# Kernel tuning notes

Hardware: AMD Instinct MI355X
Metric: run time of the kernel (lower is better)

## Reference

```python
import jax, jax.numpy as jnp
import numpy as np

BS, C, H, W = 4, 128, 64, 64  # input_dim=128
INNER = 64


def setup_inputs() -> dict:
    key = jax.random.key(0)
    ks = jax.random.split(key, 9)
    s_in = 1.0 / np.sqrt(C)
    s_inner = 1.0 / np.sqrt(INNER)
    return {
        "inpt": jax.random.normal(ks[0], (BS, C, H, W), dtype=jnp.float32),
        "Wq": jax.random.normal(ks[1], (INNER, C), dtype=jnp.float32) * s_in,
        "bq": jax.random.normal(ks[2], (INNER,), dtype=jnp.float32) * 0.01,
        "Wk": jax.random.normal(ks[3], (INNER, C), dtype=jnp.float32) * s_in,
        "bk": jax.random.normal(ks[4], (INNER,), dtype=jnp.float32) * 0.01,
        "Wv": jax.random.normal(ks[5], (INNER, C), dtype=jnp.float32) * s_in,
        "bv": jax.random.normal(ks[6], (INNER,), dtype=jnp.float32) * 0.01,
        "Wo": jax.random.normal(ks[7], (C, INNER), dtype=jnp.float32) * s_inner,
        "bo": jax.random.normal(ks[8], (C,), dtype=jnp.float32) * 0.01,
    }


def reference(inpt, Wq, bq, Wk, bk, Wv, bv, Wo, bo):
    bs, c, h, w = inpt.shape
    L = h * w
    # [bs, C, H, W] -> [bs, L, C] (tokens = spatial positions)
    x = inpt.reshape(bs, c, L).transpose(0, 2, 1)
    q = jnp.einsum('blc,dc->bld', x, Wq) + bq  # [bs, L, INNER]
    k = jnp.einsum('blc,dc->bld', x, Wk) + bk
    v = jnp.einsum('blc,dc->bld', x, Wv) + bv
    # torch code divides by np.round(sqrt(d), 2); for d=64 this is exactly 8.0
    scale = jnp.float32(np.round(np.sqrt(q.shape[-1]), 2))
    scores = jnp.einsum('bld,bmd->blm', q, k) / scale  # [bs, L, L] score matrix
    factors = jax.nn.softmax(scores, axis=-1)
    ctx = jnp.einsum('blm,bmd->bld', factors, v)  # [bs, L, INNER]
    out = jnp.einsum('bld,cd->blc', ctx, Wo) + bo  # [bs, L, C]
    out = out.transpose(0, 2, 1).reshape(bs, c, h, w)
    return inpt + out
```

## Files before the change

kernel.cpp:

```cpp
#include <hip/hip_runtime.h>
#include <hip/hip_bf16.h>

typedef __bf16 bf16x8 __attribute__((ext_vector_type(8)));
typedef __bf16 bf16x4 __attribute__((ext_vector_type(4)));
typedef short  s16x4  __attribute__((ext_vector_type(4)));
typedef float  f32x4  __attribute__((ext_vector_type(4)));

#define MFMA32(a, b, c) __builtin_amdgcn_mfma_f32_16x16x32_bf16((a), (b), (c), 0, 0, 0)
#define MFMA16K(a, b, c) __builtin_amdgcn_mfma_f32_16x16x16bf16_1k((a), (b), (c), 0, 0, 0)

#if __has_builtin(__builtin_amdgcn_exp2f)
#define EXP2F(x) __builtin_amdgcn_exp2f(x)
#else
#define EXP2F(x) __expf(0.6931471805599453f * (x))
#endif

#define GL16(G, L)                                                            \
    __builtin_amdgcn_global_load_lds(                                         \
        (const __attribute__((address_space(1))) void*)(G),                   \
        (__attribute__((address_space(3))) void*)(L), 16, 0, 0)

#define SPLIT 8
#define QSCALE 0.18033688011112042f
#define BBOUND 12.0f


__global__ __launch_bounds__(256) void qkv_kernel(
    const float* __restrict__ inpt,
    const float* __restrict__ Wq, const float* __restrict__ bq,
    const float* __restrict__ Wk, const float* __restrict__ bk,
    const float* __restrict__ Wv, const float* __restrict__ bv,
    __bf16* __restrict__ Qws, __bf16* __restrict__ Kws, __bf16* __restrict__ VTws)
{
    __shared__ __align__(16) __bf16 xT[16 * 140];
    __shared__ __align__(16) __bf16 os[16 * 144];
    const int bid = blockIdx.x;
    const int b   = bid >> 8;
    const int l0  = (bid & 255) << 4;
    const int t   = threadIdx.x;

    {
        const int c = t >> 1, half = t & 1;
        const float* xin = inpt + ((size_t)(b * 128 + c)) * 4096 + l0 + half * 8;
        float4 v0 = *(const float4*)xin;
        float4 v1 = *(const float4*)(xin + 4);
        const int tok0 = half * 8;
        xT[(tok0 + 0) * 140 + c] = (__bf16)v0.x;
        xT[(tok0 + 1) * 140 + c] = (__bf16)v0.y;
        xT[(tok0 + 2) * 140 + c] = (__bf16)v0.z;
        xT[(tok0 + 3) * 140 + c] = (__bf16)v0.w;
        xT[(tok0 + 4) * 140 + c] = (__bf16)v1.x;
        xT[(tok0 + 5) * 140 + c] = (__bf16)v1.y;
        xT[(tok0 + 6) * 140 + c] = (__bf16)v1.z;
        xT[(tok0 + 7) * 140 + c] = (__bf16)v1.w;
    }
    __syncthreads();

    const int w    = t >> 6;
    const int lane = t & 63;
    const int quad = lane >> 4;
    const int l15  = lane & 15;

    f32x4 acc[3];
    #pragma unroll
    for (int j = 0; j < 3; ++j)
        #pragma unroll
        for (int r = 0; r < 4; ++r) acc[j][r] = 0.f;

    #pragma unroll
    for (int ks = 0; ks < 4; ++ks) {
        bf16x8 af = *(const bf16x8*)&xT[l15 * 140 + ks * 32 + quad * 8];
        #pragma unroll
        for (int j = 0; j < 3; ++j) {
            const int wn   = w * 3 + j;
            const int msel = wn >> 2;
            const float* W = (msel == 0) ? Wq : ((msel == 1) ? Wk : Wv);
            const float* Wp = W + ((wn & 3) * 16 + l15) * 128 + ks * 32 + quad * 8;
            float4 wa = *(const float4*)Wp;
            float4 wb = *(const float4*)(Wp + 4);
            bf16x8 bf;
            bf[0] = (__bf16)wa.x; bf[1] = (__bf16)wa.y;
            bf[2] = (__bf16)wa.z; bf[3] = (__bf16)wa.w;
            bf[4] = (__bf16)wb.x; bf[5] = (__bf16)wb.y;
            bf[6] = (__bf16)wb.z; bf[7] = (__bf16)wb.w;
            acc[j] = MFMA32(af, bf, acc[j]);
        }
    }

    #pragma unroll
    for (int j = 0; j < 3; ++j) {
        const int wn   = w * 3 + j;
        const int msel = wn >> 2;
        const int o0   = (wn & 3) * 16;
        const float* bb = (msel == 0) ? bq : ((msel == 1) ? bk : bv);
        float bias = bb[o0 + l15];
        if (msel < 2) {
            const float scl = (msel == 0) ? QSCALE : 1.0f;
            const int oc = wn * 16 + l15;
            #pragma unroll
            for (int r = 0; r < 4; ++r)
                os[(quad * 4 + r) * 144 + oc] = (__bf16)((acc[j][r] + bias) * scl);
        } else {
            const int d  = o0 + l15;
            const int kt = l0 >> 6;
            const int kc = (l0 >> 4) & 3;
            bf16x4 v;
            #pragma unroll
            for (int r = 0; r < 4; ++r) v[r] = (__bf16)(acc[j][r] + bias);
            *(bf16x4*)(VTws + (size_t)b * 262144 + kt * 4096
                       + d * 64 + quad * 16 + kc * 4) = v;
        }
    }
    __syncthreads();

    {
        const int tok = t >> 4, c = t & 15;
        bf16x8 v = *(const bf16x8*)&os[tok * 144 + c * 8];
        if (c < 8) {
            *(bf16x8*)(Qws + ((size_t)(b * 4096 + l0 + tok)) * 64 + c * 8) = v;
        } else {
            const int d8 = c - 8;
            __bf16* dst = Kws + (size_t)b * 262144
                + (l0 >> 6) * 4096
                + ((l0 >> 4) & 3) * 1024
                + (d8 >> 2) * 512
                + (d8 & 3) * 128
                + tok * 8;
            *(bf16x8*)dst = v;
        }
    }
}

__global__ __launch_bounds__(256, 4) void attn_kernel(
    const __bf16* __restrict__ Qws, const __bf16* __restrict__ Kws,
    const __bf16* __restrict__ VTws,
    __bf16* __restrict__ Ops, float* __restrict__ Lws)
{
    __shared__ __align__(16) __bf16 sbuf[2][8192];

    const int bid   = blockIdx.x;
    const int split = bid >> 7;
    const int qi    = bid & 127;
    const int b  = qi >> 5;
    const int l0 = (qi & 31) << 7;
    const int t    = threadIdx.x;
    const int w    = t >> 6;
    const int lane = t & 63;
    const int quad = lane >> 4;
    const int l15  = lane & 15;

    bf16x8 qf[2][2];
    #pragma unroll
    for (int qs = 0; qs < 2; ++qs) {
        const __bf16* qptr = Qws
            + ((size_t)(b * 4096 + l0 + w * 32 + qs * 16 + l15)) * 64 + quad * 8;
        qf[qs][0] = *(const bf16x8*)qptr;
        qf[qs][1] = *(const bf16x8*)(qptr + 32);
    }

    f32x4 cfr[2][4];
    #pragma unroll
    for (int qs = 0; qs < 2; ++qs)
        #pragma unroll
        for (int mt = 0; mt < 4; ++mt)
            #pragma unroll
            for (int r = 0; r < 4; ++r) cfr[qs][mt][r] = 0.f;
    float l_acc[2] = {0.f, 0.f};

    int voff[8];
    #pragma unroll
    for (int mt = 0; mt < 4; ++mt) {
        const int d = mt * 16 + l15;
        #pragma unroll
        for (int kc8 = 0; kc8 < 2; ++kc8)
            voff[kc8 * 4 + mt] = d * 64 + (((2 * quad + kc8) ^ (d & 7)) * 8);
    }

    const uint4* Vg = (const uint4*)(VTws + ((size_t)b << 18));
    const int rw = t >> 3, cw = (t & 7) ^ ((t >> 3) & 7);
    const uint4* vbase = Vg + rw * 8 + cw + split * 4096;
    const uint4* kbase = (const uint4*)(Kws + ((size_t)b << 18))
                       + t + split * 4096;

    union B4 { bf16x4 h; s16x4 s; };
    union V8 { bf16x8 v; s16x4 q[2]; };

    auto stage = [&](int kt, int slot) {
        __bf16* Kd = &sbuf[slot][0];
        __bf16* Vd = &sbuf[slot][4096];
        const uint4* kp = kbase + kt * 512;
        const uint4* vp = vbase + kt * 512;
        GL16(kp,       Kd +        w * 512);
        GL16(kp + 256, Kd + 2048 + w * 512);
        GL16(vp,       Vd +        w * 512);
        GL16(vp + 256, Vd + 2048 + w * 512);
    };

    auto tile_step = [&](int slot) {
        const __bf16* Kb = &sbuf[slot][0];
        const __bf16* Vb = &sbuf[slot][4096];
        B4 pk[2][4];
        #pragma unroll
        for (int nt = 0; nt < 4; ++nt) {
            bf16x8 k0 = *(const bf16x8*)(Kb + nt * 1024 +       lane * 8);
            bf16x8 k1 = *(const bf16x8*)(Kb + nt * 1024 + 512 + lane * 8);
            #pragma unroll
            for (int qs = 0; qs < 2; ++qs) {
                f32x4 a = {-BBOUND, -BBOUND, -BBOUND, -BBOUND};
                a = MFMA32(k0, qf[qs][0], a);
                a = MFMA32(k1, qf[qs][1], a);
                float p0 = EXP2F(a[0]), p1 = EXP2F(a[1]);
                float p2 = EXP2F(a[2]), p3 = EXP2F(a[3]);
                pk[qs][nt].h[0] = (__bf16)p0; pk[qs][nt].h[1] = (__bf16)p1;
                pk[qs][nt].h[2] = (__bf16)p2; pk[qs][nt].h[3] = (__bf16)p3;
                l_acc[qs] += (p0 + p1) + (p2 + p3);
            }
        }
        __builtin_amdgcn_s_setprio(1);
        #pragma unroll
        for (int kc8 = 0; kc8 < 2; ++kc8) {
            #pragma unroll
            for (int mt = 0; mt < 4; ++mt) {
                V8 vv;
                vv.v = *(const bf16x8*)&Vb[voff[kc8 * 4 + mt]];
                #pragma unroll
                for (int qs = 0; qs < 2; ++qs) {
                    cfr[qs][mt] = MFMA16K(vv.q[0], pk[qs][2 * kc8 + 0].s, cfr[qs][mt]);
                    cfr[qs][mt] = MFMA16K(vv.q[1], pk[qs][2 * kc8 + 1].s, cfr[qs][mt]);
                }
            }
        }
        __builtin_amdgcn_s_setprio(0);
    };

    stage(0, 0);
    for (int h = 0; h < 8; ++h) {
        asm volatile("s_waitcnt vmcnt(0)" ::: "memory");
        __builtin_amdgcn_s_barrier();
        asm volatile("" ::: "memory");
        if (h < 7) stage(h + 1, (h + 1) & 1);
        tile_step(h & 1);
    }

    __builtin_amdgcn_s_barrier();
    asm volatile("" ::: "memory");

    {
        __bf16* tb = (__bf16*)sbuf + w * 2176;
        #pragma unroll
        for (int qs = 0; qs < 2; ++qs)
            #pragma unroll
            for (int mt = 0; mt < 4; ++mt) {
                bf16x4 v;
                #pragma unroll
                for (int r = 0; r < 4; ++r) v[r] = (__bf16)cfr[qs][mt][r];
                *(bf16x4*)&tb[(qs * 16 + l15) * 68 + mt * 16 + quad * 4] = v;
            }
        const int rowbase = (split * 4 + b) * 4096 + l0 + w * 32;
        #pragma unroll
        for (int hh = 0; hh < 4; ++hh) {
            const int chunk = lane + hh * 64;
            const int tok = chunk >> 3, c8 = chunk & 7;
            bf16x8 v = *(const bf16x8*)&tb[tok * 68 + c8 * 8];
            *(bf16x8*)(Ops + (size_t)(rowbase + tok) * 64 + c8 * 8) = v;
        }
        #pragma unroll
        for (int qs = 0; qs < 2; ++qs) {
            float lr = l_acc[qs];
            lr += __shfl_xor(lr, 16);
            lr += __shfl_xor(lr, 32);
            if (quad == 0) Lws[rowbase + qs * 16 + l15] = lr;
        }
    }
}

__global__ __launch_bounds__(256) void outproj_kernel(
    const float* __restrict__ inpt,
    const __bf16* __restrict__ Ops, const float* __restrict__ Lws,
    const float* __restrict__ Wo, const float* __restrict__ bo,
    float* __restrict__ out)
{
    __shared__ __align__(16) __bf16 cx[16 * 72];
    const int bid = blockIdx.x;
    const int b   = bid >> 8;
    const int l0  = (bid & 255) << 4;
    const int t   = threadIdx.x;

    {
        const int token = t >> 4, d4 = (t & 15) << 2;
        const int rowb  = b * 4096 + l0 + token;
        float denom = 0.f;
        #pragma unroll
        for (int s = 0; s < SPLIT; ++s) denom += Lws[s * 16384 + rowb];
        const float inv = 1.f / denom;
        float ax = 0.f, ay = 0.f, az = 0.f, aw = 0.f;
        #pragma unroll
        for (int s = 0; s < SPLIT; ++s) {
            const bf16x4 v = *(const bf16x4*)(Ops
                + ((size_t)(s * 16384 + rowb)) * 64 + d4);
            ax += (float)v[0]; ay += (float)v[1];
            az += (float)v[2]; aw += (float)v[3];
        }
        bf16x4 pv;
        pv[0] = (__bf16)(ax * inv); pv[1] = (__bf16)(ay * inv);
        pv[2] = (__bf16)(az * inv); pv[3] = (__bf16)(aw * inv);
        *(bf16x4*)&cx[token * 72 + d4] = pv;
    }
    __syncthreads();

    const int w    = t >> 6;
    const int lane = t & 63;
    const int quad = lane >> 4;
    const int l15  = lane & 15;

    f32x4 acc[2];
    #pragma unroll
    for (int mi = 0; mi < 2; ++mi)
        #pragma unroll
        for (int r = 0; r < 4; ++r) acc[mi][r] = 0.f;

    #pragma unroll
    for (int ks = 0; ks < 2; ++ks) {
        bf16x8 bfrag = *(const bf16x8*)&cx[l15 * 72 + ks * 32 + quad * 8];
        #pragma unroll
        for (int mi = 0; mi < 2; ++mi) {
            const int crow = (w * 2 + mi) * 16 + l15;
            const float* Wp = Wo + crow * 64 + ks * 32 + quad * 8;
            float4 wa = *(const float4*)Wp;
            float4 wb = *(const float4*)(Wp + 4);
            bf16x8 afrag;
            afrag[0] = (__bf16)wa.x; afrag[1] = (__bf16)wa.y;
            afrag[2] = (__bf16)wa.z; afrag[3] = (__bf16)wa.w;
            afrag[4] = (__bf16)wb.x; afrag[5] = (__bf16)wb.y;
            afrag[6] = (__bf16)wb.z; afrag[7] = (__bf16)wb.w;
            acc[mi] = MFMA32(afrag, bfrag, acc[mi]);
        }
    }

    #pragma unroll
    for (int mi = 0; mi < 2; ++mi) {
        #pragma unroll
        for (int r = 0; r < 4; ++r) {
            const int c = (w * 2 + mi) * 16 + quad * 4 + r;
            const size_t addr = ((size_t)(b * 128 + c)) * 4096 + l0 + l15;
            out[addr] = inpt[addr] + bo[c] + acc[mi][r];
        }
    }
}

extern "C" void kernel_launch(void* const* d_in, const int* in_sizes, int n_in,
                              void* d_out, int out_size, void* d_ws, size_t ws_size,
                              hipStream_t stream)
{
    const float* inpt = (const float*)d_in[0];
    const float* Wq   = (const float*)d_in[1];
    const float* bq   = (const float*)d_in[2];
    const float* Wk   = (const float*)d_in[3];
    const float* bk   = (const float*)d_in[4];
    const float* Wv   = (const float*)d_in[5];
    const float* bv   = (const float*)d_in[6];
    const float* Wo   = (const float*)d_in[7];
    const float* bo   = (const float*)d_in[8];
    float* out = (float*)d_out;

    char* ws = (char*)d_ws;
    const size_t MB = (size_t)1 << 20;
    __bf16* Qws  = (__bf16*)(ws + 0 * MB);
    __bf16* Kws  = (__bf16*)(ws + 2 * MB);
    __bf16* VTws = (__bf16*)(ws + 4 * MB);
    __bf16* Ops  = (__bf16*)(ws + 6 * MB);
    float*  Lws  = (float*)(ws + 24 * MB);

    qkv_kernel<<<1024, 256, 0, stream>>>(inpt, Wq, bq, Wk, bk, Wv, bv, Qws, Kws, VTws);
    attn_kernel<<<SPLIT * 128, 256, 0, stream>>>(Qws, Kws, VTws, Ops, Lws);
    outproj_kernel<<<1024, 256, 0, stream>>>(inpt, Ops, Lws, Wo, bo, out);
}
```

Before: 125.0 us.

## Pre-convert weights to bf16 and enlarge QKV/outproj token tiles to 64

Adds a small kernel that converts Wq/Wk/Wv/Wo to bf16 once per call into the workspace. The QKV and output-projection kernels now process 64 tokens per block instead of 16, so each weight fragment is reused across four token tiles rather than being reloaded and converted from fp32 per block. Grid sizes drop from 1024 to 256 blocks, which increases per-thread register use (12 accumulators in QKV) and adds an extra launch, at the risk of lower parallelism on a large GPU.

After: 118.5 us. 5.2% less time.

```diff
diff --git a/kernel.cpp b/kernel.cpp
--- a/kernel.cpp
+++ b/kernel.cpp
@@ -25,34 +25,51 @@
 #define BBOUND 12.0f
 
 
-__global__ __launch_bounds__(256) void qkv_kernel(
+__global__ __launch_bounds__(256) void wprep_kernel(
+    const float* __restrict__ Wq, const float* __restrict__ Wk,
+    const float* __restrict__ Wv, const float* __restrict__ Wo,
+    __bf16* __restrict__ Wqkv_b, __bf16* __restrict__ Wo_b)
+{
+    const int idx = (blockIdx.x * 256 + threadIdx.x) * 4;
+    const float* src;
+    __bf16* dst;
+    if (idx < 8192)       { src = Wq + idx;         dst = Wqkv_b + idx; }
+    else if (idx < 16384) { src = Wk + idx - 8192;  dst = Wqkv_b + idx; }
+    else if (idx < 24576) { src = Wv + idx - 16384; dst = Wqkv_b + idx; }
+    else                  { src = Wo + idx - 24576; dst = Wo_b + idx - 24576; }
+    float4 v = *(const float4*)src;
+    bf16x4 o;
+    o[0] = (__bf16)v.x; o[1] = (__bf16)v.y;
+    o[2] = (__bf16)v.z; o[3] = (__bf16)v.w;
+    *(bf16x4*)dst = o;
+}
+
+__global__ __launch_bounds__(256, 4) void qkv_kernel(
     const float* __restrict__ inpt,
-    const float* __restrict__ Wq, const float* __restrict__ bq,
-    const float* __restrict__ Wk, const float* __restrict__ bk,
-    const float* __restrict__ Wv, const float* __restrict__ bv,
+    const float* __restrict__ bq, const float* __restrict__ bk,
+    const float* __restrict__ bv,
+    const __bf16* __restrict__ Wqkv_b,
     __bf16* __restrict__ Qws, __bf16* __restrict__ Kws, __bf16* __restrict__ VTws)
 {
-    __shared__ __align__(16) __bf16 xT[16 * 140];
-    __shared__ __align__(16) __bf16 os[16 * 144];
+    __shared__ __align__(16) __bf16 xT[64 * 136];
+    __shared__ __align__(16) __bf16 os[64 * 136];
     const int bid = blockIdx.x;
-    const int b   = bid >> 8;
-    const int l0  = (bid & 255) << 4;
+    const int b   = bid >> 6;
+    const int l0  = (bid & 63) << 6;
     const int t   = threadIdx.x;
 
     {
         const int c = t >> 1, half = t & 1;
-        const float* xin = inpt + ((size_t)(b * 128 + c)) * 4096 + l0 + half * 8;
-        float4 v0 = *(const float4*)xin;
-        float4 v1 = *(const float4*)(xin + 4);
-        const int tok0 = half * 8;
-        xT[(tok0 + 0) * 140 + c] = (__bf16)v0.x;
-        xT[(tok0 + 1) * 140 + c] = (__bf16)v0.y;
-        xT[(tok0 + 2) * 140 + c] = (__bf16)v0.z;
-        xT[(tok0 + 3) * 140 + c] = (__bf16)v0.w;
-        xT[(tok0 + 4) * 140 + c] = (__bf16)v1.x;
-        xT[(tok0 + 5) * 140 + c] = (__bf16)v1.y;
-        xT[(tok0 + 6) * 140 + c] = (__bf16)v1.z;
-        xT[(tok0 + 7) * 140 + c] = (__bf16)v1.w;
+        const float* xin = inpt + ((size_t)(b * 128 + c)) * 4096 + l0 + half * 32;
+        #pragma unroll
+        for (int i = 0; i < 8; ++i) {
+            float4 v = *(const float4*)(xin + i * 4);
+            const int tok = half * 32 + i * 4;
+            xT[(tok + 0) * 136 + c] = (__bf16)v.x;
+            xT[(tok + 1) * 136 + c] = (__bf16)v.y;
+            xT[(tok + 2) * 136 + c] = (__bf16)v.z;
+            xT[(tok + 3) * 136 + c] = (__bf16)v.w;
+        }
     }
     __syncthreads();
 
@@ -61,71 +78,63 @@
     const int quad = lane >> 4;
     const int l15  = lane & 15;
 
-    f32x4 acc[3];
-    #pragma unroll
-    for (int j = 0; j < 3; ++j)
+    f32x4 acc[12];
+    #pragma unroll
+    for (int j = 0; j < 12; ++j)
         #pragma unroll
         for (int r = 0; r < 4; ++r) acc[j][r] = 0.f;
 
     #pragma unroll
     for (int ks = 0; ks < 4; ++ks) {
-        bf16x8 af = *(const bf16x8*)&xT[l15 * 140 + ks * 32 + quad * 8];
-        #pragma unroll
-        for (int j = 0; j < 3; ++j) {
-            const int wn   = w * 3 + j;
-            const int msel = wn >> 2;
-            const float* W = (msel == 0) ? Wq : ((msel == 1) ? Wk : Wv);
-            const float* Wp = W + ((wn & 3) * 16 + l15) * 128 + ks * 32 + quad * 8;
-            float4 wa = *(const float4*)Wp;
-            float4 wb = *(const float4*)(Wp + 4);
-            bf16x8 bf;
-            bf[0] = (__bf16)wa.x; bf[1] = (__bf16)wa.y;
-            bf[2] = (__bf16)wa.z; bf[3] = (__bf16)wa.w;
-            bf[4] = (__bf16)wb.x; bf[5] = (__bf16)wb.y;
-            bf[6] = (__bf16)wb.z; bf[7] = (__bf16)wb.w;
+        bf16x8 af = *(const bf16x8*)&xT[(w * 16 + l15) * 136 + ks * 32 + quad * 8];
+        #pragma unroll
+        for (int j = 0; j < 12; ++j) {
+            bf16x8 bf = *(const bf16x8*)(Wqkv_b + j * 2048 + l15 * 128
+                                         + ks * 32 + quad * 8);
             acc[j] = MFMA32(af, bf, acc[j]);
         }
     }
 
     #pragma unroll
-    for (int j = 0; j < 3; ++j) {
-        const int wn   = w * 3 + j;
-        const int msel = wn >> 2;
-        const int o0   = (wn & 3) * 16;
+    for (int j = 0; j < 12; ++j) {
+        const int msel = j >> 2;
+        const int o0   = (j & 3) * 16;
         const float* bb = (msel == 0) ? bq : ((msel == 1) ? bk : bv);
         float bias = bb[o0 + l15];
         if (msel < 2) {
             const float scl = (msel == 0) ? QSCALE : 1.0f;
-            const int oc = wn * 16 + l15;
+            const int oc = j * 16 + l15;
             #pragma unroll
             for (int r = 0; r < 4; ++r)
-                os[(quad * 4 + r) * 144 + oc] = (__bf16)((acc[j][r] + bias) * scl);
+                os[(w * 16 + quad * 4 + r) * 136 + oc]
+                    = (__bf16)((acc[j][r] + bias) * scl);
         } else {
             const int d  = o0 + l15;
-            const int kt = l0 >> 6;
-            const int kc = (l0 >> 4) & 3;
+            const int kt = bid & 63;
             bf16x4 v;
             #pragma unroll
             for (int r = 0; r < 4; ++r) v[r] = (__bf16)(acc[j][r] + bias);
             *(bf16x4*)(VTws + (size_t)b * 262144 + kt * 4096
-                       + d * 64 + quad * 16 + kc * 4) = v;
+                       + d * 64 + quad * 16 + w * 4) = v;
         }
     }
     __syncthreads();
 
-    {
-        const int tok = t >> 4, c = t & 15;
-        bf16x8 v = *(const bf16x8*)&os[tok * 144 + c * 8];
-        if (c < 8) {
-            *(bf16x8*)(Qws + ((size_t)(b * 4096 + l0 + tok)) * 64 + c * 8) = v;
+    #pragma unroll
+    for (int g = 0; g < 4; ++g) {
+        const int cid = t + g * 256;
+        const int tok = cid >> 4, c8 = cid & 15;
+        bf16x8 v = *(const bf16x8*)&os[tok * 136 + c8 * 8];
+        if (c8 < 8) {
+            *(bf16x8*)(Qws + ((size_t)(b * 4096 + l0 + tok)) * 64 + c8 * 8) = v;
         } else {
-            const int d8 = c - 8;
+            const int d8 = c8 - 8;
             __bf16* dst = Kws + (size_t)b * 262144
-                + (l0 >> 6) * 4096
-                + ((l0 >> 4) & 3) * 1024
+                + (bid & 63) * 4096
+                + (tok >> 4) * 1024
                 + (d8 >> 2) * 512
                 + (d8 & 3) * 128
-                + tok * 8;
+                + (tok & 15) * 8;
             *(bf16x8*)dst = v;
         }
     }
@@ -274,37 +283,41 @@
     }
 }
 
-__global__ __launch_bounds__(256) void outproj_kernel(
+__global__ __launch_bounds__(256, 4) void outproj_kernel(
     const float* __restrict__ inpt,
     const __bf16* __restrict__ Ops, const float* __restrict__ Lws,
-    const float* __restrict__ Wo, const float* __restrict__ bo,
+    const __bf16* __restrict__ Wo_b, const float* __restrict__ bo,
     float* __restrict__ out)
 {
-    __shared__ __align__(16) __bf16 cx[16 * 72];
+    __shared__ __align__(16) __bf16 cx[64 * 72];
     const int bid = blockIdx.x;
-    const int b   = bid >> 8;
-    const int l0  = (bid & 255) << 4;
+    const int b   = bid >> 6;
+    const int l0  = (bid & 63) << 6;
     const int t   = threadIdx.x;
 
     {
-        const int token = t >> 4, d4 = (t & 15) << 2;
+        const int token = t >> 2;
         const int rowb  = b * 4096 + l0 + token;
         float denom = 0.f;
         #pragma unroll
         for (int s = 0; s < SPLIT; ++s) denom += Lws[s * 16384 + rowb];
         const float inv = 1.f / denom;
-        float ax = 0.f, ay = 0.f, az = 0.f, aw = 0.f;
-        #pragma unroll
-        for (int s = 0; s < SPLIT; ++s) {
-            const bf16x4 v = *(const bf16x4*)(Ops
-                + ((size_t)(s * 16384 + rowb)) * 64 + d4);
-            ax += (float)v[0]; ay += (float)v[1];
-            az += (float)v[2]; aw += (float)v[3];
-        }
-        bf16x4 pv;
-        pv[0] = (__bf16)(ax * inv); pv[1] = (__bf16)(ay * inv);
-        pv[2] = (__bf16)(az * inv); pv[3] = (__bf16)(aw * inv);
-        *(bf16x4*)&cx[token * 72 + d4] = pv;
+        #pragma unroll
+        for (int g = 0; g < 4; ++g) {
+            const int d4 = (((t & 3) + g * 4)) << 2;
+            float ax = 0.f, ay = 0.f, az = 0.f, aw = 0.f;
+            #pragma unroll
+            for (int s = 0; s < SPLIT; ++s) {
+                const bf16x4 v = *(const bf16x4*)(Ops
+                    + ((size_t)(s * 16384 + rowb)) * 64 + d4);
+                ax += (float)v[0]; ay += (float)v[1];
+                az += (float)v[2]; aw += (float)v[3];
+            }
+            bf16x4 pv;
+            pv[0] = (__bf16)(ax * inv); pv[1] = (__bf16)(ay * inv);
+            pv[2] = (__bf16)(az * inv); pv[3] = (__bf16)(aw * inv);
+            *(bf16x4*)&cx[token * 72 + d4] = pv;
+        }
     }
     __syncthreads();
 
@@ -313,37 +326,42 @@
     const int quad = lane >> 4;
     const int l15  = lane & 15;
 
-    f32x4 acc[2];
+    f32x4 acc[2][4];
     #pragma unroll
     for (int mi = 0; mi < 2; ++mi)
         #pragma unroll
-        for (int r = 0; r < 4; ++r) acc[mi][r] = 0.f;
+        for (int nt = 0; nt < 4; ++nt)
+            #pragma unroll
+            for (int r = 0; r < 4; ++r) acc[mi][nt][r] = 0.f;
 
     #pragma unroll
     for (int ks = 0; ks < 2; ++ks) {
-        bf16x8 bfrag = *(const bf16x8*)&cx[l15 * 72 + ks * 32 + quad * 8];
+        bf16x8 bfr[4];
+        #pragma unroll
+        for (int nt = 0; nt < 4; ++nt)
+            bfr[nt] = *(const bf16x8*)&cx[(nt * 16 + l15) * 72 + ks * 32 + quad * 8];
         #pragma unroll
         for (int mi = 0; mi < 2; ++mi) {
             const int crow = (w * 2 + mi) * 16 + l15;
-            const float* Wp = Wo + crow * 64 + ks * 32 + quad * 8;
-            float4 wa = *(const float4*)Wp;
-            float4 wb = *(const float4*)(Wp + 4);
-            bf16x8 afrag;
-            afrag[0] = (__bf16)wa.x; afrag[1] = (__bf16)wa.y;
-            afrag[2] = (__bf16)wa.z; afrag[3] = (__bf16)wa.w;
-            afrag[4] = (__bf16)wb.x; afrag[5] = (__bf16)wb.y;
-            afrag[6] = (__bf16)wb.z; afrag[7] = (__bf16)wb.w;
-            acc[mi] = MFMA32(afrag, bfrag, acc[mi]);
+            bf16x8 af = *(const bf16x8*)(Wo_b + crow * 64 + ks * 32 + quad * 8);
+            #pragma unroll
+            for (int nt = 0; nt < 4; ++nt)
+                acc[mi][nt] = MFMA32(af, bfr[nt], acc[mi][nt]);
         }
     }
 
     #pragma unroll
     for (int mi = 0; mi < 2; ++mi) {
-        #pragma unroll
-        for (int r = 0; r < 4; ++r) {
-            const int c = (w * 2 + mi) * 16 + quad * 4 + r;
-            const size_t addr = ((size_t)(b * 128 + c)) * 4096 + l0 + l15;
-            out[addr] = inpt[addr] + bo[c] + acc[mi][r];
+        const int c0 = (w * 2 + mi) * 16 + quad * 4;
+        #pragma unroll
+        for (int nt = 0; nt < 4; ++nt) {
+            #pragma unroll
+            for (int r = 0; r < 4; ++r) {
+                const int c = c0 + r;
+                const size_t addr = ((size_t)(b * 128 + c)) * 4096
+                                  + l0 + nt * 16 + l15;
+                out[addr] = inpt[addr] + bo[c] + acc[mi][nt][r];
+            }
         }
     }
 }
@@ -365,13 +383,16 @@
 
     char* ws = (char*)d_ws;
     const size_t MB = (size_t)1 << 20;
-    __bf16* Qws  = (__bf16*)(ws + 0 * MB);
-    __bf16* Kws  = (__bf16*)(ws + 2 * MB);
-    __bf16* VTws = (__bf16*)(ws + 4 * MB);
-    __bf16* Ops  = (__bf16*)(ws + 6 * MB);
-    float*  Lws  = (float*)(ws + 24 * MB);
-
-    qkv_kernel<<<1024, 256, 0, stream>>>(inpt, Wq, bq, Wk, bk, Wv, bv, Qws, Kws, VTws);
+    __bf16* Qws    = (__bf16*)(ws + 0 * MB);
+    __bf16* Kws    = (__bf16*)(ws + 2 * MB);
+    __bf16* VTws   = (__bf16*)(ws + 4 * MB);
+    __bf16* Ops    = (__bf16*)(ws + 6 * MB);
+    float*  Lws    = (float*)(ws + 24 * MB);
+    __bf16* Wqkv_b = (__bf16*)(ws + 25 * MB);
+    __bf16* Wo_b   = (__bf16*)(ws + 25 * MB + (64 << 10));
+
+    wprep_kernel<<<32, 256, 0, stream>>>(Wq, Wk, Wv, Wo, Wqkv_b, Wo_b);
+    qkv_kernel<<<256, 256, 0, stream>>>(inpt, bq, bk, bv, Wqkv_b, Qws, Kws, VTws);
     attn_kernel<<<SPLIT * 128, 256, 0, stream>>>(Qws, Kws, VTws, Ops, Lws);
-    outproj_kernel<<<1024, 256, 0, stream>>>(inpt, Ops, Lws, Wo, bo, out);
-}
+    outproj_kernel<<<256, 256, 0, stream>>>(inpt, Ops, Lws, Wo_b, bo, out);
+}
```
